# Performance work log

Measured on AMD Instinct MI355X. Metric: run time of the kernel, lower is better.

The kernel has to match this reference:

```python
import jax, jax.numpy as jnp
import numpy as np

N_NODES = 100000
N_EDGES = 1600000
D = 128
N_LAYERS = 3
N_GRAPHS = 128


def setup_inputs() -> dict:
    key = jax.random.key(0)
    ks = jax.random.split(key, 8)
    x = jax.random.normal(ks[0], (N_NODES, D), dtype=jnp.float32)
    # stacked GIN-MLP params (all layers are D->D since hidden_dim == in_dim)
    scale = 1.0 / np.sqrt(D)
    W1 = jax.random.normal(ks[1], (N_LAYERS, D, D), dtype=jnp.float32) * scale
    b1 = jax.random.normal(ks[2], (N_LAYERS, D), dtype=jnp.float32) * 0.01
    W2 = jax.random.normal(ks[3], (N_LAYERS, D, D), dtype=jnp.float32) * scale
    b2 = jax.random.normal(ks[4], (N_LAYERS, D), dtype=jnp.float32) * 0.01
    edge_index = jax.random.randint(ks[5], (2, N_EDGES), 0, N_NODES, dtype=jnp.int64)
    batch = jnp.sort(jax.random.randint(ks[6], (N_NODES,), 0, N_GRAPHS, dtype=jnp.int64))
    return {"x": x, "W1": W1, "b1": b1, "W2": W2, "b2": b2,
            "edge_index": edge_index, "batch": batch}


def reference(x, W1, b1, W2, b2, edge_index, batch):
    src = edge_index[0]
    dst = edge_index[1]
    n = x.shape[0]
    eps = jnp.float32(0.0)  # GIN eps (PyG default, not trained)
    for i in range(N_LAYERS):
        # gather neighbor features along edges, scatter-add to destination nodes
        agg = jax.ops.segment_sum(x[src], dst, num_segments=n)  # [N, D]
        h = (1.0 + eps) * x + agg
        h = jax.nn.relu(h @ W1[i] + b1[i])
        x = h @ W2[i] + b2[i]
    # sum-pool readout per graph
    h_G = jax.ops.segment_sum(x, batch, num_segments=N_GRAPHS)  # [G, D]
    return h_G
```

## Files before the change

### kernel.cpp

```cpp
#include <hip/hip_runtime.h>
#include <hip/hip_bf16.h>
#include <stdint.h>

#define N_NODES 100000
#define N_EDGES 1600000
#define DIM 128
#define N_GRAPHS 128
#define LDA 136

#define NBKT 392
#define BCAP 6144
#define BP   5632
#define IDXCAP 2048

#define NBIN_BLK 391
#define CVT_BLK 3125

typedef unsigned int uint32;
typedef unsigned short ushort16;

typedef __bf16 bf16x8 __attribute__((ext_vector_type(8)));
typedef float fx4 __attribute__((ext_vector_type(4)));

__device__ __forceinline__ float bfLo(uint32 u){ return __builtin_bit_cast(float, (uint32)(u << 16)); }
__device__ __forceinline__ float bfHi(uint32 u){ return __builtin_bit_cast(float, (uint32)(u & 0xFFFF0000u)); }
__device__ __forceinline__ ushort16 f2bf(float f){
  uint32 u = __builtin_bit_cast(uint32, f);
  u = u + 0x7FFFu + ((u >> 16) & 1u);
  return (ushort16)(u >> 16);
}
__device__ __forceinline__ uint32 pack2(float a, float b){
  return (uint32)f2bf(a) | ((uint32)f2bf(b) << 16);
}

__global__ __launch_bounds__(512) void k_prep(const float* __restrict__ x,
                                              const float* __restrict__ W1, const float* __restrict__ W2,
                                              const int* __restrict__ ei,
                                              ushort16* __restrict__ P, ushort16* __restrict__ Q,
                                              ushort16* __restrict__ Wf,
                                              int* __restrict__ bucketCursor,
                                              int* __restrict__ temp){
  __shared__ int hist[NBKT];
  __shared__ int base[NBKT];
  __shared__ int gbase[NBKT];
  __shared__ int scanbuf[512];
  __shared__ int sVal[4096];
  __shared__ unsigned short sBkt[4096];

  int bb = blockIdx.x;
  int t  = threadIdx.x;

  if (bb < NBIN_BLK){
    int e0 = bb * 4096;
    for (int i = t; i < NBKT; i += 512) hist[i] = 0;
    __syncthreads();

    int   myv[8];
    short myb[8];
    short myr[8];
    #pragma unroll
    for (int it = 0; it < 8; ++it){
      int e = e0 + it*512 + t;
      int v = 0; short b = -1; short r = 0;
      if (e < N_EDGES){
        int s = ei[e];
        int d = ei[N_EDGES + e];
        b = (short)(d >> 8);
        v = s | ((d & 255) << 17);
        r = (short)atomicAdd(&hist[b], 1);
      }
      myv[it] = v; myb[it] = b; myr[it] = r;
    }
    __syncthreads();

    scanbuf[t] = (t < NBKT) ? hist[t] : 0;
    __syncthreads();
    for (int off = 1; off < 512; off <<= 1){
      int x2 = 0;
      if (t >= off) x2 = scanbuf[t - off];
      __syncthreads();
      scanbuf[t] += x2;
      __syncthreads();
    }
    if (t < NBKT){
      base[t]  = scanbuf[t] - hist[t];
      gbase[t] = atomicAdd(&bucketCursor[t], hist[t]);
    }
    __syncthreads();

    #pragma unroll
    for (int it = 0; it < 8; ++it){
      if (myb[it] >= 0){
        int p = base[myb[it]] + myr[it];
        sVal[p] = myv[it];
        sBkt[p] = (unsigned short)myb[it];
      }
    }
    __syncthreads();

    int cnt = scanbuf[NBKT - 1];
    for (int p = t; p < cnt; p += 512){
      int b = sBkt[p];
      int g = gbase[b] + (p - base[b]);
      if (g < BCAP) temp[b*BCAP + g] = sVal[p];
    }
    return;
  }

  if (bb < NBIN_BLK + CVT_BLK){
    int idx = ((bb - NBIN_BLK)*512 + t) * 8;
    float4 v0 = *(const float4*)(x + idx);
    float4 v1 = *(const float4*)(x + idx + 4);
    uint4 o;
    o.x = pack2(v0.x, v0.y); o.y = pack2(v0.z, v0.w);
    o.z = pack2(v1.x, v1.y); o.w = pack2(v1.z, v1.w);
    *(uint4*)(P + idx) = o;
    return;
  }

  if (bb == NBIN_BLK + CVT_BLK){
    uint4 z = {0u,0u,0u,0u};
    if (t < 16)                *(uint4*)(P + (size_t)N_NODES*128 + t*8)      = z;
    else if (t < 32)           *(uint4*)(Q + (size_t)N_NODES*128 + (t-16)*8) = z;
    return;
  }

  int tid = (bb - (NBIN_BLK + CVT_BLK + 1))*512 + t;
  int layer = tid >> 12;
  int rem   = tid & 4095;
  int mat   = rem >> 11;
  int nt    = (rem >> 8) & 7;
  int kt    = (rem >> 6) & 3;
  int lane  = rem & 63;
  int kg = lane >> 4, m = lane & 15;
  int n  = nt*16 + m;
  int kb = kt*32 + kg*8;
  const float* src = (mat ? W2 : W1) + layer*16384;
  uint4 o;
  o.x = pack2(src[(kb+0)*128 + n], src[(kb+1)*128 + n]);
  o.y = pack2(src[(kb+2)*128 + n], src[(kb+3)*128 + n]);
  o.z = pack2(src[(kb+4)*128 + n], src[(kb+5)*128 + n]);
  o.w = pack2(src[(kb+6)*128 + n], src[(kb+7)*128 + n]);
  *(uint4*)(Wf + ((((size_t)(layer*2+mat)*8 + nt)*4 + kt)*64 + lane)*8) = o;
}

__global__ __launch_bounds__(512) void k_binB(const int* __restrict__ temp,
                                              const int* __restrict__ bucketCursor,
                                              int* __restrict__ rowptr,
                                              int* __restrict__ rowlen,
                                              int* __restrict__ colx){
  __shared__ int counts[256];
  __shared__ int sc[256];
  __shared__ int cur[256];
  __shared__ int stage[BCAP];
  __shared__ int sorted[BCAP];
  int b = blockIdx.x, t = threadIdx.x;
  int cnt = min(bucketCursor[b], BCAP);
  int gb  = b * BP;
  const int* src = temp + b*BCAP;

  if (t < 256) counts[t] = 0;
  __syncthreads();
  for (int p = t; p < cnt; p += 512){
    int v = src[p];
    stage[p] = v;
    atomicAdd(&counts[v >> 17], 1);
  }
  __syncthreads();

  int len = 0, plen = 0;
  if (t < 256){
    len  = counts[t];
    plen = (len + 3) & ~3;
    sc[t] = plen;
  }
  __syncthreads();
  for (int off = 1; off < 256; off <<= 1){
    int x = 0;
    if (t < 256 && t >= off) x = sc[t - off];
    __syncthreads();
    if (t < 256) sc[t] += x;
    __syncthreads();
  }
  int excl = 0;
  if (t < 256){
    excl = sc[t] - plen;
    cur[t] = excl;
    int node = b*256 + t;
    if (node < N_NODES){ rowptr[node] = gb + excl; rowlen[node] = plen; }
  }
  __syncthreads();

  for (int p = t; p < cnt; p += 512){
    int v = stage[p];
    int d = v >> 17;
    int pos = atomicAdd(&cur[d], 1);
    sorted[pos] = v & 0x1FFFF;
  }
  __syncthreads();

  if (t < 256){
    for (int k = len; k < plen; ++k) sorted[excl + k] = N_NODES;
  }
  __syncthreads();

  int total = min(sc[255], BP);
  for (int p = t; p < total; p += 512) colx[gb + p] = sorted[p];
}

template<bool LAST>
__global__ __launch_bounds__(256, 6) void k_gin(const ushort16* __restrict__ xb, ushort16* __restrict__ hb,
                                                const ushort16* __restrict__ Wt1, const float* __restrict__ b1,
                                                const ushort16* __restrict__ Wt2, const float* __restrict__ b2,
                                                const int* __restrict__ rowptr, const int* __restrict__ rowlen,
                                                const int* __restrict__ colx,
                                                const int* __restrict__ batch, float* __restrict__ outp){
  __shared__ __attribute__((aligned(16))) ushort16 sA[64 * LDA];
  __shared__ __attribute__((aligned(16))) int sIdx[IDXCAP];
  __shared__ int sOff[64];
  __shared__ int sLen[64];
  __shared__ int sBat[64];

  int t = threadIdx.x;
  int row0 = blockIdx.x * 64;
  int jBase = rowptr[row0];
  int lastV = min(row0 + 63, N_NODES - 1);
  int total = rowptr[lastV] + rowlen[lastV] - jBase;

  if (t < 64){
    int gg = row0 + t;
    int off = 0, len = 0;
    if (gg < N_NODES){ off = rowptr[gg] - jBase; len = rowlen[gg]; }
    sOff[t] = off; sLen[t] = len;
    if (LAST) sBat[t] = (gg < N_NODES) ? batch[gg] : 0;
  }
  bool fast = (total <= IDXCAP);
  if (fast){
    for (int p = t; p < total; p += 256) sIdx[p] = colx[jBase + p];
  }
  __syncthreads();

  int wave = t >> 6, lane = t & 63;
  int g16 = lane >> 4, o = lane & 15;
  const uint32* xw = (const uint32*)xb;

#define GATH(r) (*(const uint4*)(xw + (size_t)(r)*64 + o*4))
#define ACC8(u) do { \
    a0 += (fx4){ bfLo((u).x), bfHi((u).x), bfLo((u).y), bfHi((u).y) }; \
    a1 += (fx4){ bfLo((u).z), bfHi((u).z), bfLo((u).w), bfHi((u).w) }; \
  } while(0)

  for (int q = 0; q < 4; ++q){
    int ln  = wave*16 + q*4 + g16;
    int off = sOff[ln];
    int len = sLen[ln];
    int gn  = row0 + ln;
    uint4 xv = {0u,0u,0u,0u};
    if (gn < N_NODES) xv = *(const uint4*)(xw + (size_t)gn*64 + o*4);
    fx4 a0 = (fx4){0.f,0.f,0.f,0.f};
    fx4 a1 = (fx4){0.f,0.f,0.f,0.f};

    if (fast){
      int rd = 0;
      for (; rd + 8 <= len; rd += 8){
        int i0 = sIdx[off+rd  ], i1 = sIdx[off+rd+1], i2 = sIdx[off+rd+2], i3 = sIdx[off+rd+3];
        int i4 = sIdx[off+rd+4], i5 = sIdx[off+rd+5], i6 = sIdx[off+rd+6], i7 = sIdx[off+rd+7];
        uint4 u0 = GATH(i0); uint4 u1 = GATH(i1); uint4 u2 = GATH(i2); uint4 u3 = GATH(i3);
        uint4 u4 = GATH(i4); uint4 u5 = GATH(i5); uint4 u6 = GATH(i6); uint4 u7 = GATH(i7);
        ACC8(u0); ACC8(u1); ACC8(u2); ACC8(u3);
        ACC8(u4); ACC8(u5); ACC8(u6); ACC8(u7);
      }
      if (rd < len){
        int i0 = sIdx[off+rd], i1 = sIdx[off+rd+1], i2 = sIdx[off+rd+2], i3 = sIdx[off+rd+3];
        uint4 u0 = GATH(i0); uint4 u1 = GATH(i1); uint4 u2 = GATH(i2); uint4 u3 = GATH(i3);
        ACC8(u0); ACC8(u1); ACC8(u2); ACC8(u3);
      }
    } else {
      for (int rd = 0; rd < len; rd += 4){
        int i0 = colx[jBase+off+rd], i1 = colx[jBase+off+rd+1];
        int i2 = colx[jBase+off+rd+2], i3 = colx[jBase+off+rd+3];
        uint4 u0 = GATH(i0); uint4 u1 = GATH(i1); uint4 u2 = GATH(i2); uint4 u3 = GATH(i3);
        ACC8(u0); ACC8(u1); ACC8(u2); ACC8(u3);
      }
    }

    uint4 r;
    r.x = pack2(a0[0]+bfLo(xv.x), a0[1]+bfHi(xv.x));
    r.y = pack2(a0[2]+bfLo(xv.y), a0[3]+bfHi(xv.y));
    r.z = pack2(a1[0]+bfLo(xv.z), a1[1]+bfHi(xv.z));
    r.w = pack2(a1[2]+bfLo(xv.w), a1[3]+bfHi(xv.w));
    *(uint4*)(sA + ln*LDA + o*8) = r;
  }
#undef GATH
#undef ACC8
  __syncthreads();

  int m = lane & 15, kg = lane >> 4;
  int n0 = wave * 2;

  bf16x8 bfa[4], bfb[4];
  #pragma unroll
  for (int kt = 0; kt < 4; ++kt){
    bfa[kt] = *(const bf16x8*)(Wt1 + (((n0+0)*4 + kt)*64 + lane)*8);
    bfb[kt] = *(const bf16x8*)(Wt1 + (((n0+1)*4 + kt)*64 + lane)*8);
  }

  fx4 acc[4][2];
  #pragma unroll
  for (int mt = 0; mt < 4; ++mt){ acc[mt][0] = (fx4){0,0,0,0}; acc[mt][1] = (fx4){0,0,0,0}; }

  #pragma unroll
  for (int kt = 0; kt < 4; ++kt){
    #pragma unroll
    for (int mt = 0; mt < 4; ++mt){
      bf16x8 av = *(const bf16x8*)(sA + (mt*16 + m)*LDA + kg*8 + kt*32);
      acc[mt][0] = __builtin_amdgcn_mfma_f32_16x16x32_bf16(av, bfa[kt], acc[mt][0], 0, 0, 0);
      acc[mt][1] = __builtin_amdgcn_mfma_f32_16x16x32_bf16(av, bfb[kt], acc[mt][1], 0, 0, 0);
    }
  }
  float bva = b1[(n0+0)*16 + m];
  float bvb = b1[(n0+1)*16 + m];
  __syncthreads();

  #pragma unroll
  for (int mt = 0; mt < 4; ++mt){
    #pragma unroll
    for (int r = 0; r < 4; ++r){
      int row = mt*16 + kg*4 + r;
      sA[row*LDA + (n0+0)*16 + m] = f2bf(fmaxf(acc[mt][0][r] + bva, 0.f));
      sA[row*LDA + (n0+1)*16 + m] = f2bf(fmaxf(acc[mt][1][r] + bvb, 0.f));
    }
  }
  #pragma unroll
  for (int kt = 0; kt < 4; ++kt){
    bfa[kt] = *(const bf16x8*)(Wt2 + (((n0+0)*4 + kt)*64 + lane)*8);
    bfb[kt] = *(const bf16x8*)(Wt2 + (((n0+1)*4 + kt)*64 + lane)*8);
  }
  float cva = b2[(n0+0)*16 + m];
  float cvb = b2[(n0+1)*16 + m];
  #pragma unroll
  for (int mt = 0; mt < 4; ++mt){ acc[mt][0] = (fx4){0,0,0,0}; acc[mt][1] = (fx4){0,0,0,0}; }
  __syncthreads();

  #pragma unroll
  for (int kt = 0; kt < 4; ++kt){
    #pragma unroll
    for (int mt = 0; mt < 4; ++mt){
      bf16x8 av = *(const bf16x8*)(sA + (mt*16 + m)*LDA + kg*8 + kt*32);
      acc[mt][0] = __builtin_amdgcn_mfma_f32_16x16x32_bf16(av, bfa[kt], acc[mt][0], 0, 0, 0);
      acc[mt][1] = __builtin_amdgcn_mfma_f32_16x16x32_bf16(av, bfb[kt], acc[mt][1], 0, 0, 0);
    }
  }

  if constexpr (!LAST){
    #pragma unroll
    for (int mt = 0; mt < 4; ++mt){
      #pragma unroll
      for (int r = 0; r < 4; ++r){
        int row = row0 + mt*16 + kg*4 + r;
        if (row < N_NODES){
          hb[row*128 + (n0+0)*16 + m] = f2bf(acc[mt][0][r] + cva);
          hb[row*128 + (n0+1)*16 + m] = f2bf(acc[mt][1][r] + cvb);
        }
      }
    }
  } else {
    float sum0 = 0.f, sum1 = 0.f; int curg = -1;
    #pragma unroll
    for (int mt = 0; mt < 4; ++mt){
      #pragma unroll
      for (int r = 0; r < 4; ++r){
        int lrow = mt*16 + kg*4 + r;
        int grow = row0 + lrow;
        if (grow < N_NODES){
          int gg = sBat[lrow];
          if (gg != curg){
            if (curg >= 0){
              atomicAdd(&outp[curg*128 + (n0+0)*16 + m], sum0);
              atomicAdd(&outp[curg*128 + (n0+1)*16 + m], sum1);
            }
            curg = gg; sum0 = 0.f; sum1 = 0.f;
          }
          sum0 += acc[mt][0][r] + cva;
          sum1 += acc[mt][1][r] + cvb;
        }
      }
    }
    if (curg >= 0){
      atomicAdd(&outp[curg*128 + (n0+0)*16 + m], sum0);
      atomicAdd(&outp[curg*128 + (n0+1)*16 + m], sum1);
    }
  }
}

extern "C" void kernel_launch(void* const* d_in, const int* in_sizes, int n_in,
                              void* d_out, int out_size, void* d_ws, size_t ws_size,
                              hipStream_t stream) {
  const float* x   = (const float*)d_in[0];
  const float* W1  = (const float*)d_in[1];
  const float* b1  = (const float*)d_in[2];
  const float* W2  = (const float*)d_in[3];
  const float* b2  = (const float*)d_in[4];
  const int*   ei  = (const int*)d_in[5];
  const int*   bat = (const int*)d_in[6];
  float* out = (float*)d_out;

  char* w = (char*)d_ws;
  auto carve = [&](size_t bytes) -> char* {
    char* p = w; w += (bytes + 255) & ~(size_t)255; return p;
  };
  ushort16* P    = (ushort16*)carve((size_t)(N_NODES+1) * DIM * 2);
  ushort16* Q    = (ushort16*)carve((size_t)(N_NODES+1) * DIM * 2);
  ushort16* Wf   = (ushort16*)carve((size_t)3 * 2 * 16384 * 2);
  int* rowptr    = (int*)carve((size_t)N_NODES * 4);
  int* rowlen    = (int*)carve((size_t)N_NODES * 4);
  int* colx      = (int*)carve((size_t)NBKT * BP * 4);
  int* bucketCursor = (int*)carve((NBKT + 1) * 4);
  int* temp      = (int*)Q;

  hipMemsetAsync(bucketCursor, 0, (NBKT + 1) * 4, stream);
  hipMemsetAsync(d_out, 0, (size_t)N_GRAPHS * DIM * 4, stream);

  k_prep<<<NBIN_BLK + CVT_BLK + 1 + 24, 512, 0, stream>>>(x, W1, W2, ei, P, Q, Wf,
                                                          bucketCursor, temp);
  k_binB<<<NBKT, 512, 0, stream>>>(temp, bucketCursor, rowptr, rowlen, colx);

  const int ginGrid = (N_NODES + 63) / 64;

  k_gin<false><<<ginGrid, 256, 0, stream>>>(P, Q, Wf + 0*16384, b1 + 0*128, Wf + 1*16384, b2 + 0*128,
                                            rowptr, rowlen, colx, bat, out);
  k_gin<false><<<ginGrid, 256, 0, stream>>>(Q, P, Wf + 2*16384, b1 + 1*128, Wf + 3*16384, b2 + 1*128,
                                            rowptr, rowlen, colx, bat, out);
  k_gin<true><<<ginGrid, 256, 0, stream>>>(P, Q, Wf + 4*16384, b1 + 2*128, Wf + 5*16384, b2 + 2*128,
                                           rowptr, rowlen, colx, bat, out);
}
```

Measured before the change: 325.7 us.

## Bin edges per 64-node tile and fuse CSR build into first GIN layer

Edges are now binned directly by 64-node tile (1563 tiles), not 256-node buckets, so the separate second-stage sort kernel is removed. The first GIN layer sorts its tile's edges in shared memory, writes rowptr/rowlen/colx for later layers, and uses the sorted indices immediately. The slow global-index fallback path is dropped because each tile's index list always fits in shared memory. The cost is more global atomics on tile cursors and a fixed per-tile cap of 1536 edges, which could overflow on skewed graphs.

```diff
diff --git a/kernel.cpp b/kernel.cpp
--- a/kernel.cpp
+++ b/kernel.cpp
@@ -8,10 +8,8 @@
 #define N_GRAPHS 128
 #define LDA 136
 
-#define NBKT 392
-#define BCAP 6144
-#define BP   5632
-#define IDXCAP 2048
+#define NTILE 1563
+#define TCAP 1536
 
 #define NBIN_BLK 391
 #define CVT_BLK 3125
@@ -38,11 +36,11 @@
                                               const int* __restrict__ ei,
                                               ushort16* __restrict__ P, ushort16* __restrict__ Q,
                                               ushort16* __restrict__ Wf,
-                                              int* __restrict__ bucketCursor,
-                                              int* __restrict__ temp){
-  __shared__ int hist[NBKT];
-  __shared__ int base[NBKT];
-  __shared__ int gbase[NBKT];
+                                              int* __restrict__ tileCursor,
+                                              int* __restrict__ colx){
+  __shared__ int hist[NTILE];
+  __shared__ int base[NTILE];
+  __shared__ int gbase[NTILE];
   __shared__ int scanbuf[512];
   __shared__ int sVal[4096];
   __shared__ unsigned short sBkt[4096];
@@ -52,7 +50,7 @@
 
   if (bb < NBIN_BLK){
     int e0 = bb * 4096;
-    for (int i = t; i < NBKT; i += 512) hist[i] = 0;
+    for (int i = t; i < NTILE; i += 512) hist[i] = 0;
     __syncthreads();
 
     int   myv[8];
@@ -65,27 +63,42 @@
       if (e < N_EDGES){
         int s = ei[e];
         int d = ei[N_EDGES + e];
-        b = (short)(d >> 8);
-        v = s | ((d & 255) << 17);
+        b = (short)(d >> 6);
+        v = s | ((d & 63) << 17);
         r = (short)atomicAdd(&hist[b], 1);
       }
       myv[it] = v; myb[it] = b; myr[it] = r;
     }
     __syncthreads();
 
-    scanbuf[t] = (t < NBKT) ? hist[t] : 0;
+    int c0, c1, c2, c3, sum;
+    {
+      int i0 = 4*t;
+      c0 = (i0+0 < NTILE) ? hist[i0+0] : 0;
+      c1 = (i0+1 < NTILE) ? hist[i0+1] : 0;
+      c2 = (i0+2 < NTILE) ? hist[i0+2] : 0;
+      c3 = (i0+3 < NTILE) ? hist[i0+3] : 0;
+      sum = c0 + c1 + c2 + c3;
+    }
+    scanbuf[t] = sum;
     __syncthreads();
     for (int off = 1; off < 512; off <<= 1){
-      int x2 = 0;
-      if (t >= off) x2 = scanbuf[t - off];
+      int x2 = (t >= off) ? scanbuf[t - off] : 0;
       __syncthreads();
       scanbuf[t] += x2;
       __syncthreads();
     }
-    if (t < NBKT){
-      base[t]  = scanbuf[t] - hist[t];
-      gbase[t] = atomicAdd(&bucketCursor[t], hist[t]);
-    }
+    {
+      int ex = scanbuf[t] - sum;
+      int i0 = 4*t;
+      if (i0+0 < NTILE) base[i0+0] = ex;
+      if (i0+1 < NTILE) base[i0+1] = ex + c0;
+      if (i0+2 < NTILE) base[i0+2] = ex + c0 + c1;
+      if (i0+3 < NTILE) base[i0+3] = ex + c0 + c1 + c2;
+    }
+    __syncthreads();
+
+    for (int i = t; i < NTILE; i += 512) gbase[i] = atomicAdd(&tileCursor[i], hist[i]);
     __syncthreads();
 
     #pragma unroll
@@ -98,11 +111,11 @@
     }
     __syncthreads();
 
-    int cnt = scanbuf[NBKT - 1];
+    int cnt = scanbuf[511];
     for (int p = t; p < cnt; p += 512){
       int b = sBkt[p];
       int g = gbase[b] + (p - base[b]);
-      if (g < BCAP) temp[b*BCAP + g] = sVal[p];
+      if (g < TCAP) colx[b*TCAP + g] = sVal[p];
     }
     return;
   }
@@ -144,101 +157,88 @@
   *(uint4*)(Wf + ((((size_t)(layer*2+mat)*8 + nt)*4 + kt)*64 + lane)*8) = o;
 }
 
-__global__ __launch_bounds__(512) void k_binB(const int* __restrict__ temp,
-                                              const int* __restrict__ bucketCursor,
-                                              int* __restrict__ rowptr,
-                                              int* __restrict__ rowlen,
-                                              int* __restrict__ colx){
-  __shared__ int counts[256];
-  __shared__ int sc[256];
-  __shared__ int cur[256];
-  __shared__ int stage[BCAP];
-  __shared__ int sorted[BCAP];
-  int b = blockIdx.x, t = threadIdx.x;
-  int cnt = min(bucketCursor[b], BCAP);
-  int gb  = b * BP;
-  const int* src = temp + b*BCAP;
-
-  if (t < 256) counts[t] = 0;
-  __syncthreads();
-  for (int p = t; p < cnt; p += 512){
-    int v = src[p];
-    stage[p] = v;
-    atomicAdd(&counts[v >> 17], 1);
-  }
-  __syncthreads();
-
-  int len = 0, plen = 0;
-  if (t < 256){
-    len  = counts[t];
-    plen = (len + 3) & ~3;
-    sc[t] = plen;
-  }
-  __syncthreads();
-  for (int off = 1; off < 256; off <<= 1){
-    int x = 0;
-    if (t < 256 && t >= off) x = sc[t - off];
-    __syncthreads();
-    if (t < 256) sc[t] += x;
-    __syncthreads();
-  }
-  int excl = 0;
-  if (t < 256){
-    excl = sc[t] - plen;
-    cur[t] = excl;
-    int node = b*256 + t;
-    if (node < N_NODES){ rowptr[node] = gb + excl; rowlen[node] = plen; }
-  }
-  __syncthreads();
-
-  for (int p = t; p < cnt; p += 512){
-    int v = stage[p];
-    int d = v >> 17;
-    int pos = atomicAdd(&cur[d], 1);
-    sorted[pos] = v & 0x1FFFF;
-  }
-  __syncthreads();
-
-  if (t < 256){
-    for (int k = len; k < plen; ++k) sorted[excl + k] = N_NODES;
-  }
-  __syncthreads();
-
-  int total = min(sc[255], BP);
-  for (int p = t; p < total; p += 512) colx[gb + p] = sorted[p];
-}
-
-template<bool LAST>
+template<bool BUILD, bool LAST>
 __global__ __launch_bounds__(256, 6) void k_gin(const ushort16* __restrict__ xb, ushort16* __restrict__ hb,
                                                 const ushort16* __restrict__ Wt1, const float* __restrict__ b1,
                                                 const ushort16* __restrict__ Wt2, const float* __restrict__ b2,
-                                                const int* __restrict__ rowptr, const int* __restrict__ rowlen,
-                                                const int* __restrict__ colx,
+                                                int* __restrict__ rowptr, int* __restrict__ rowlen,
+                                                int* __restrict__ colx, const int* __restrict__ tileCursor,
                                                 const int* __restrict__ batch, float* __restrict__ outp){
   __shared__ __attribute__((aligned(16))) ushort16 sA[64 * LDA];
-  __shared__ __attribute__((aligned(16))) int sIdx[IDXCAP];
+  __shared__ __attribute__((aligned(16))) int sIdx[TCAP];
   __shared__ int sOff[64];
   __shared__ int sLen[64];
+  __shared__ int sCur[64];
   __shared__ int sBat[64];
 
   int t = threadIdx.x;
-  int row0 = blockIdx.x * 64;
-  int jBase = rowptr[row0];
-  int lastV = min(row0 + 63, N_NODES - 1);
-  int total = rowptr[lastV] + rowlen[lastV] - jBase;
-
-  if (t < 64){
-    int gg = row0 + t;
-    int off = 0, len = 0;
-    if (gg < N_NODES){ off = rowptr[gg] - jBase; len = rowlen[gg]; }
-    sOff[t] = off; sLen[t] = len;
-    if (LAST) sBat[t] = (gg < N_NODES) ? batch[gg] : 0;
-  }
-  bool fast = (total <= IDXCAP);
-  if (fast){
+  int tb = blockIdx.x;
+  int row0 = tb * 64;
+  int jBase = tb * TCAP;
+
+  if (BUILD){
+    int* stage = (int*)sA;
+    int cnt = min(tileCursor[tb], TCAP);
+    if (t < 64) sLen[t] = 0;
+    __syncthreads();
+    for (int p = t; p < cnt; p += 256) stage[p] = colx[jBase + p];
+    __syncthreads();
+    for (int p = t; p < cnt; p += 256) atomicAdd(&sLen[stage[p] >> 17], 1);
+    __syncthreads();
+
+    int len = 0, plen = 0;
+    if (t < 64){ len = sLen[t]; plen = (len + 3) & ~3; sCur[t] = plen; }
+    __syncthreads();
+    for (int off = 1; off < 64; off <<= 1){
+      int x = 0;
+      if (t < 64 && t >= off) x = sCur[t - off];
+      __syncthreads();
+      if (t < 64) sCur[t] += x;
+      __syncthreads();
+    }
+    int excl = 0;
+    if (t < 64){
+      excl = sCur[t] - plen;
+      sOff[t] = excl;
+      sLen[t] = plen;
+      int node = row0 + t;
+      if (node < N_NODES){ rowptr[node] = jBase + excl; rowlen[node] = plen; }
+      if (LAST) sBat[t] = (node < N_NODES) ? batch[node] : 0;
+    }
+    __syncthreads();
+    if (t < 64) sCur[t] = excl;
+    __syncthreads();
+
+    for (int p = t; p < cnt; p += 256){
+      int v = stage[p];
+      int d = v >> 17;
+      int pos = atomicAdd(&sCur[d], 1);
+      if (pos < TCAP) sIdx[pos] = v & 0x1FFFF;
+    }
+    __syncthreads();
+    if (t < 64){
+      for (int k = len; k < plen; ++k){
+        int p = excl + k;
+        if (p < TCAP) sIdx[p] = N_NODES;
+      }
+    }
+    __syncthreads();
+
+    int total = min(sOff[63] + sLen[63], TCAP);
+    for (int p = t; p < total; p += 256) colx[jBase + p] = sIdx[p];
+  } else {
+    if (t < 64){
+      int gg = row0 + t;
+      int off = 0, len = 0;
+      if (gg < N_NODES){ off = rowptr[gg] - jBase; len = rowlen[gg]; }
+      sOff[t] = off; sLen[t] = len;
+      if (LAST) sBat[t] = (gg < N_NODES) ? batch[gg] : 0;
+    }
+    int lastV = min(row0 + 63, N_NODES - 1);
+    int total = min(rowptr[lastV] + rowlen[lastV] - jBase, TCAP);
     for (int p = t; p < total; p += 256) sIdx[p] = colx[jBase + p];
-  }
-  __syncthreads();
+    __syncthreads();
+  }
 
   int wave = t >> 6, lane = t & 63;
   int g16 = lane >> 4, o = lane & 15;
@@ -260,28 +260,19 @@
     fx4 a0 = (fx4){0.f,0.f,0.f,0.f};
     fx4 a1 = (fx4){0.f,0.f,0.f,0.f};
 
-    if (fast){
-      int rd = 0;
-      for (; rd + 8 <= len; rd += 8){
-        int i0 = sIdx[off+rd  ], i1 = sIdx[off+rd+1], i2 = sIdx[off+rd+2], i3 = sIdx[off+rd+3];
-        int i4 = sIdx[off+rd+4], i5 = sIdx[off+rd+5], i6 = sIdx[off+rd+6], i7 = sIdx[off+rd+7];
-        uint4 u0 = GATH(i0); uint4 u1 = GATH(i1); uint4 u2 = GATH(i2); uint4 u3 = GATH(i3);
-        uint4 u4 = GATH(i4); uint4 u5 = GATH(i5); uint4 u6 = GATH(i6); uint4 u7 = GATH(i7);
-        ACC8(u0); ACC8(u1); ACC8(u2); ACC8(u3);
-        ACC8(u4); ACC8(u5); ACC8(u6); ACC8(u7);
-      }
-      if (rd < len){
-        int i0 = sIdx[off+rd], i1 = sIdx[off+rd+1], i2 = sIdx[off+rd+2], i3 = sIdx[off+rd+3];
-        uint4 u0 = GATH(i0); uint4 u1 = GATH(i1); uint4 u2 = GATH(i2); uint4 u3 = GATH(i3);
-        ACC8(u0); ACC8(u1); ACC8(u2); ACC8(u3);
-      }
-    } else {
-      for (int rd = 0; rd < len; rd += 4){
-        int i0 = colx[jBase+off+rd], i1 = colx[jBase+off+rd+1];
-        int i2 = colx[jBase+off+rd+2], i3 = colx[jBase+off+rd+3];
-        uint4 u0 = GATH(i0); uint4 u1 = GATH(i1); uint4 u2 = GATH(i2); uint4 u3 = GATH(i3);
-        ACC8(u0); ACC8(u1); ACC8(u2); ACC8(u3);
-      }
+    int rd = 0;
+    for (; rd + 8 <= len; rd += 8){
+      int i0 = sIdx[off+rd  ], i1 = sIdx[off+rd+1], i2 = sIdx[off+rd+2], i3 = sIdx[off+rd+3];
+      int i4 = sIdx[off+rd+4], i5 = sIdx[off+rd+5], i6 = sIdx[off+rd+6], i7 = sIdx[off+rd+7];
+      uint4 u0 = GATH(i0); uint4 u1 = GATH(i1); uint4 u2 = GATH(i2); uint4 u3 = GATH(i3);
+      uint4 u4 = GATH(i4); uint4 u5 = GATH(i5); uint4 u6 = GATH(i6); uint4 u7 = GATH(i7);
+      ACC8(u0); ACC8(u1); ACC8(u2); ACC8(u3);
+      ACC8(u4); ACC8(u5); ACC8(u6); ACC8(u7);
+    }
+    if (rd < len){
+      int i0 = sIdx[off+rd], i1 = sIdx[off+rd+1], i2 = sIdx[off+rd+2], i3 = sIdx[off+rd+3];
+      uint4 u0 = GATH(i0); uint4 u1 = GATH(i1); uint4 u2 = GATH(i2); uint4 u3 = GATH(i3);
+      ACC8(u0); ACC8(u1); ACC8(u2); ACC8(u3);
     }
 
     uint4 r;
@@ -414,23 +405,21 @@
   ushort16* Wf   = (ushort16*)carve((size_t)3 * 2 * 16384 * 2);
   int* rowptr    = (int*)carve((size_t)N_NODES * 4);
   int* rowlen    = (int*)carve((size_t)N_NODES * 4);
-  int* colx      = (int*)carve((size_t)NBKT * BP * 4);
-  int* bucketCursor = (int*)carve((NBKT + 1) * 4);
-  int* temp      = (int*)Q;
-
-  hipMemsetAsync(bucketCursor, 0, (NBKT + 1) * 4, stream);
+  int* colx      = (int*)carve((size_t)NTILE * TCAP * 4);
+  int* tileCursor = (int*)carve((NTILE + 1) * 4);
+
+  hipMemsetAsync(tileCursor, 0, (NTILE + 1) * 4, stream);
   hipMemsetAsync(d_out, 0, (size_t)N_GRAPHS * DIM * 4, stream);
 
   k_prep<<<NBIN_BLK + CVT_BLK + 1 + 24, 512, 0, stream>>>(x, W1, W2, ei, P, Q, Wf,
-                                                          bucketCursor, temp);
-  k_binB<<<NBKT, 512, 0, stream>>>(temp, bucketCursor, rowptr, rowlen, colx);
-
-  const int ginGrid = (N_NODES + 63) / 64;
-
-  k_gin<false><<<ginGrid, 256, 0, stream>>>(P, Q, Wf + 0*16384, b1 + 0*128, Wf + 1*16384, b2 + 0*128,
-                                            rowptr, rowlen, colx, bat, out);
-  k_gin<false><<<ginGrid, 256, 0, stream>>>(Q, P, Wf + 2*16384, b1 + 1*128, Wf + 3*16384, b2 + 1*128,
-                                            rowptr, rowlen, colx, bat, out);
-  k_gin<true><<<ginGrid, 256, 0, stream>>>(P, Q, Wf + 4*16384, b1 + 2*128, Wf + 5*16384, b2 + 2*128,
-                                           rowptr, rowlen, colx, bat, out);
+                                                          tileCursor, colx);
+
+  const int ginGrid = NTILE;
+
+  k_gin<true,  false><<<ginGrid, 256, 0, stream>>>(P, Q, Wf + 0*16384, b1 + 0*128, Wf + 1*16384, b2 + 0*128,
+                                                   rowptr, rowlen, colx, tileCursor, bat, out);
+  k_gin<false, false><<<ginGrid, 256, 0, stream>>>(Q, P, Wf + 2*16384, b1 + 1*128, Wf + 3*16384, b2 + 1*128,
+                                                   rowptr, rowlen, colx, tileCursor, bat, out);
+  k_gin<false, true ><<<ginGrid, 256, 0, stream>>>(P, Q, Wf + 4*16384, b1 + 2*128, Wf + 5*16384, b2 + 2*128,
+                                                   rowptr, rowlen, colx, tileCursor, bat, out);
 }
```

New measurement: 326.9 us. Within noise of the previous version (+0.3%).
